# Performance work log

Hardware: AMD Instinct MI355X
Metric: run time of the kernel (lower is better)

## Reference

```python
import jax, jax.numpy as jnp
import numpy as np

NUM_BREAKPOINTS = 100  # module default
IMG_SHAPE = (1, 1, 4096, 8192)  # B must be 1: PWL(num_channels=1) sees (C*H*W, B)


def setup_inputs() -> dict:
    key = jax.random.key(0)
    k1, k2, k3, k4 = jax.random.split(key, 4)
    x = jax.random.uniform(k1, IMG_SHAPE, dtype=jnp.float32)
    # torchpwl.PWL parameters (num_channels=1): breakpoint x-positions, per-segment
    # slopes, and bias (function value at the leftmost breakpoint).
    x_positions = jax.random.uniform(k2, (1, NUM_BREAKPOINTS), dtype=jnp.float32)
    slopes = 1.0 + 0.1 * jax.random.normal(k3, (1, NUM_BREAKPOINTS), dtype=jnp.float32)
    biases = 0.05 * jax.random.normal(k4, (1,), dtype=jnp.float32)
    return {"x": x, "x_positions": x_positions, "slopes": slopes, "biases": biases}


def _pwl(x_flat, x_positions, slopes, biases):
    # Sloped piecewise-linear function (torchpwl.BaseSlopedPWL math), 1 channel.
    # x_flat: (N,), x_positions/slopes: (1, K), biases: (1,)
    K = x_positions.shape[1]
    sorted_x = jnp.sort(x_positions, axis=1)                     # (1, K)
    skips = jnp.roll(sorted_x, -1, axis=1) - sorted_x            # last entry never used
    cumsums = jnp.cumsum(skips * slopes, axis=1)[:, :-1]         # (1, K-1)
    betas = jnp.concatenate([biases[:, None], biases[:, None] + cumsums], axis=1)  # (1, K)
    # segment index: (# breakpoints <= x) clamped to [1, K], minus 1
    idx = jnp.clip(jnp.searchsorted(sorted_x[0], x_flat, side="right"), 1, K) - 1
    return betas[0, idx] + (x_flat - sorted_x[0, idx]) * slopes[0, idx]


def reference(x, x_positions, slopes, biases):
    # forward: flatten -> PWL -> clip(0,1) -> reshape (original returns [out])
    y = _pwl(x.reshape(-1), x_positions, slopes, biases)
    return jnp.clip(y, 0.0, 1.0).reshape(x.shape)
```

## Files before the change

### kernel.cpp

```cpp
#include <hip/hip_runtime.h>

#define K  100
#define NB 1024

typedef float fvec4 __attribute__((ext_vector_type(4)));

__global__ __launch_bounds__(1024) void pwl_setup_kernel(
    const float* __restrict__ xp, const float* __restrict__ sl,
    const float* __restrict__ bias, float2* __restrict__ bab_g,
    float* __restrict__ sx_g, float2* __restrict__ ab_g) {
  __shared__ float s_pos[K];
  __shared__ float s_slope[K];
  __shared__ float s_sorted[K];
  __shared__ float s_a[K];
  __shared__ float s_b[K];
  __shared__ unsigned short s_cnt[NB + 1];
  const int t = threadIdx.x;

  if (t < K) { s_pos[t] = xp[t]; s_slope[t] = sl[t]; }
  __syncthreads();

  if (t < K) {
    float v = s_pos[t];
    int r = 0;
    for (int j = 0; j < K; ++j) {
      float u = s_pos[j];
      r += ((u < v) || (u == v && j < t)) ? 1 : 0;
    }
    s_sorted[r] = v;
  }
  __syncthreads();

  if (t == 0) {
    float acc = bias[0];
    for (int i = 0; i < K; ++i) {
      if (i) acc += (s_sorted[i] - s_sorted[i - 1]) * s_slope[i - 1];
      float a = s_slope[i];
      s_a[i] = a;
      s_b[i] = acc - s_sorted[i] * a;
    }
  }
  __syncthreads();

  if (t < K) {
    sx_g[t] = s_sorted[t];
    ab_g[t] = make_float2(s_a[t], s_b[t]);
  }

  for (int e = t; e <= NB; e += blockDim.x) {
    float ev = (float)e * (1.0f / (float)NB);
    int c = 0;
    for (int j = 0; j < K; ++j) c += (s_sorted[j] <= ev) ? 1 : 0;
    s_cnt[e] = (unsigned short)c;
  }
  __syncthreads();

  for (int b = t; b < NB; b += blockDim.x) {
    int lo = s_cnt[b], hi = s_cnt[b + 1];
    float2 e;
    if (lo == hi) {
      int idx = min(max(lo, 1), K) - 1;
      e = make_float2(s_a[idx], s_b[idx]);
    } else {
      e.x = __builtin_huge_valf();
      e.y = __uint_as_float((unsigned)lo | ((unsigned)hi << 16));
    }
    bab_g[b] = e;
  }
}

__device__ __forceinline__ float pwl_eval(float xv,
                                          const float2* __restrict__ s_bab,
                                          const float* __restrict__ s_x,
                                          const float2* __restrict__ s_ab) {
  int b = (int)(xv * (float)NB);
  b = min(max(b, 0), NB - 1);
  float2 ab = s_bab[b];
  if (__float_as_uint(ab.x) == 0x7f800000u) {
    unsigned p = __float_as_uint(ab.y);
    int lo = (int)(p & 0xffffu);
    int hi = (int)(p >> 16);
    while (lo < hi) {
      int mid = (lo + hi) >> 1;
      if (s_x[mid] <= xv) lo = mid + 1; else hi = mid;
    }
    int idx = min(max(lo, 1), K) - 1;
    ab = s_ab[idx];
  }
  float y = fmaf(xv, ab.x, ab.y);
  return fminf(fmaxf(y, 0.0f), 1.0f);
}

__global__ __launch_bounds__(256) void pwl_main_kernel(
    const fvec4* __restrict__ x, const float2* __restrict__ bab_g,
    const float* __restrict__ sx_g, const float2* __restrict__ ab_g,
    fvec4* __restrict__ out, int n4, int n) {
  __shared__ float2 s_bab[NB];
  __shared__ float s_x[K];
  __shared__ float2 s_ab[K];
  for (int i = threadIdx.x; i < NB; i += blockDim.x) s_bab[i] = bab_g[i];
  if (threadIdx.x < K) {
    s_x[threadIdx.x] = sx_g[threadIdx.x];
    s_ab[threadIdx.x] = ab_g[threadIdx.x];
  }
  __syncthreads();

  const int stride = gridDim.x * blockDim.x;
  int i = blockIdx.x * blockDim.x + threadIdx.x;
  if (i < n4) {
    fvec4 v = __builtin_nontemporal_load(&x[i]);
    while (true) {
      int inext = i + stride;
      bool more = inext < n4;
      fvec4 vn = {};
      if (more) vn = __builtin_nontemporal_load(&x[inext]);
      fvec4 r;
      r.x = pwl_eval(v.x, s_bab, s_x, s_ab);
      r.y = pwl_eval(v.y, s_bab, s_x, s_ab);
      r.z = pwl_eval(v.z, s_bab, s_x, s_ab);
      r.w = pwl_eval(v.w, s_bab, s_x, s_ab);
      __builtin_nontemporal_store(r, &out[i]);
      if (!more) break;
      v = vn;
      i = inext;
    }
  }

  if (blockIdx.x == 0) {
    const float* xs = (const float*)x;
    float* os = (float*)out;
    for (int j = (n4 << 2) + threadIdx.x; j < n; j += blockDim.x) {
      os[j] = pwl_eval(xs[j], s_bab, s_x, s_ab);
    }
  }
}

extern "C" void kernel_launch(void* const* d_in, const int* in_sizes, int n_in,
                              void* d_out, int out_size, void* d_ws, size_t ws_size,
                              hipStream_t stream) {
  const float* x    = (const float*)d_in[0];
  const float* xp   = (const float*)d_in[1];
  const float* sl   = (const float*)d_in[2];
  const float* bias = (const float*)d_in[3];
  float* out = (float*)d_out;

  float2* bab = (float2*)d_ws;
  float* sx   = (float*)((char*)d_ws + NB * 8);
  float2* ab  = (float2*)((char*)d_ws + NB * 8 + 512);

  const int n  = in_sizes[0];
  const int n4 = n >> 2;

  pwl_setup_kernel<<<1, 1024, 0, stream>>>(xp, sl, bias, bab, sx, ab);

  const int threads = 256;
  const int blocks  = 2048;
  pwl_main_kernel<<<blocks, threads, 0, stream>>>(
      (const fvec4*)x, bab, sx, ab, (fvec4*)out, n4, n);
}
```

Baseline: 238.8 us.

## Fuse PWL table setup into main kernel, recomputed per block

Removes the separate single-block setup kernel. Each block of the main kernel now sorts the breakpoints, builds the bucket table in shared memory and then streams the data. The serial prefix sum is replaced by a parallel scan, and the bucket counting uses binary search instead of a linear scan. The launch changes to 1024 blocks of 512 threads. This saves a kernel launch and its dependency gap, but every block repeats the setup work before it starts streaming.

```diff
diff --git a/kernel.cpp b/kernel.cpp
--- a/kernel.cpp
+++ b/kernel.cpp
@@ -1,73 +1,11 @@
 #include <hip/hip_runtime.h>
 
-#define K  100
-#define NB 1024
+#define K   100
+#define NB  1024
+#define BS  512
+#define NBLK 1024
 
 typedef float fvec4 __attribute__((ext_vector_type(4)));
-
-__global__ __launch_bounds__(1024) void pwl_setup_kernel(
-    const float* __restrict__ xp, const float* __restrict__ sl,
-    const float* __restrict__ bias, float2* __restrict__ bab_g,
-    float* __restrict__ sx_g, float2* __restrict__ ab_g) {
-  __shared__ float s_pos[K];
-  __shared__ float s_slope[K];
-  __shared__ float s_sorted[K];
-  __shared__ float s_a[K];
-  __shared__ float s_b[K];
-  __shared__ unsigned short s_cnt[NB + 1];
-  const int t = threadIdx.x;
-
-  if (t < K) { s_pos[t] = xp[t]; s_slope[t] = sl[t]; }
-  __syncthreads();
-
-  if (t < K) {
-    float v = s_pos[t];
-    int r = 0;
-    for (int j = 0; j < K; ++j) {
-      float u = s_pos[j];
-      r += ((u < v) || (u == v && j < t)) ? 1 : 0;
-    }
-    s_sorted[r] = v;
-  }
-  __syncthreads();
-
-  if (t == 0) {
-    float acc = bias[0];
-    for (int i = 0; i < K; ++i) {
-      if (i) acc += (s_sorted[i] - s_sorted[i - 1]) * s_slope[i - 1];
-      float a = s_slope[i];
-      s_a[i] = a;
-      s_b[i] = acc - s_sorted[i] * a;
-    }
-  }
-  __syncthreads();
-
-  if (t < K) {
-    sx_g[t] = s_sorted[t];
-    ab_g[t] = make_float2(s_a[t], s_b[t]);
-  }
-
-  for (int e = t; e <= NB; e += blockDim.x) {
-    float ev = (float)e * (1.0f / (float)NB);
-    int c = 0;
-    for (int j = 0; j < K; ++j) c += (s_sorted[j] <= ev) ? 1 : 0;
-    s_cnt[e] = (unsigned short)c;
-  }
-  __syncthreads();
-
-  for (int b = t; b < NB; b += blockDim.x) {
-    int lo = s_cnt[b], hi = s_cnt[b + 1];
-    float2 e;
-    if (lo == hi) {
-      int idx = min(max(lo, 1), K) - 1;
-      e = make_float2(s_a[idx], s_b[idx]);
-    } else {
-      e.x = __builtin_huge_valf();
-      e.y = __uint_as_float((unsigned)lo | ((unsigned)hi << 16));
-    }
-    bab_g[b] = e;
-  }
-}
 
 __device__ __forceinline__ float pwl_eval(float xv,
                                           const float2* __restrict__ s_bab,
@@ -91,22 +29,77 @@
   return fminf(fmaxf(y, 0.0f), 1.0f);
 }
 
-__global__ __launch_bounds__(256) void pwl_main_kernel(
-    const fvec4* __restrict__ x, const float2* __restrict__ bab_g,
-    const float* __restrict__ sx_g, const float2* __restrict__ ab_g,
+__global__ __launch_bounds__(BS) void pwl_fused_kernel(
+    const fvec4* __restrict__ x, const float* __restrict__ xp,
+    const float* __restrict__ sl, const float* __restrict__ bias,
     fvec4* __restrict__ out, int n4, int n) {
+  __shared__ float s_pos[K];
+  __shared__ float s_slope[K];
+  __shared__ float s_x[K];
+  __shared__ float s_c[K];
+  __shared__ float2 s_ab[K];
+  __shared__ unsigned short s_cnt[NB + 1];
   __shared__ float2 s_bab[NB];
-  __shared__ float s_x[K];
-  __shared__ float2 s_ab[K];
-  for (int i = threadIdx.x; i < NB; i += blockDim.x) s_bab[i] = bab_g[i];
-  if (threadIdx.x < K) {
-    s_x[threadIdx.x] = sx_g[threadIdx.x];
-    s_ab[threadIdx.x] = ab_g[threadIdx.x];
+
+  const int t = threadIdx.x;
+
+  if (t < K) { s_pos[t] = xp[t]; s_slope[t] = sl[t]; }
+  __syncthreads();
+
+  if (t < K) {
+    float v = s_pos[t];
+    int r = 0;
+    for (int j = 0; j < K; ++j) {
+      float u = s_pos[j];
+      r += ((u < v) || (u == v && j < t)) ? 1 : 0;
+    }
+    s_x[r] = v;
   }
   __syncthreads();
 
-  const int stride = gridDim.x * blockDim.x;
-  int i = blockIdx.x * blockDim.x + threadIdx.x;
+  if (t < K - 1) s_c[t] = (s_x[t + 1] - s_x[t]) * s_slope[t];
+  __syncthreads();
+  for (int off = 1; off < K - 1; off <<= 1) {
+    float v = 0.0f;
+    if (t >= off && t < K - 1) v = s_c[t - off];
+    __syncthreads();
+    if (t < K - 1) s_c[t] += v;
+    __syncthreads();
+  }
+  if (t < K) {
+    float beta = bias[0] + (t ? s_c[t - 1] : 0.0f);
+    float a = s_slope[t];
+    s_ab[t] = make_float2(a, beta - s_x[t] * a);
+  }
+  __syncthreads();
+
+  for (int e = t; e <= NB; e += BS) {
+    float ev = (float)e * (1.0f / (float)NB);
+    int lo = 0, hi = K;
+    while (lo < hi) {
+      int mid = (lo + hi) >> 1;
+      if (s_x[mid] <= ev) lo = mid + 1; else hi = mid;
+    }
+    s_cnt[e] = (unsigned short)lo;
+  }
+  __syncthreads();
+
+  for (int b = t; b < NB; b += BS) {
+    int lo = s_cnt[b], hi = s_cnt[b + 1];
+    float2 e;
+    if (lo == hi) {
+      int idx = min(max(lo, 1), K) - 1;
+      e = s_ab[idx];
+    } else {
+      e.x = __builtin_huge_valf();
+      e.y = __uint_as_float((unsigned)lo | ((unsigned)hi << 16));
+    }
+    s_bab[b] = e;
+  }
+  __syncthreads();
+
+  const int stride = NBLK * BS;
+  int i = blockIdx.x * BS + t;
   if (i < n4) {
     fvec4 v = __builtin_nontemporal_load(&x[i]);
     while (true) {
@@ -129,7 +122,7 @@
   if (blockIdx.x == 0) {
     const float* xs = (const float*)x;
     float* os = (float*)out;
-    for (int j = (n4 << 2) + threadIdx.x; j < n; j += blockDim.x) {
+    for (int j = (n4 << 2) + t; j < n; j += BS) {
       os[j] = pwl_eval(xs[j], s_bab, s_x, s_ab);
     }
   }
@@ -144,17 +137,9 @@
   const float* bias = (const float*)d_in[3];
   float* out = (float*)d_out;
 
-  float2* bab = (float2*)d_ws;
-  float* sx   = (float*)((char*)d_ws + NB * 8);
-  float2* ab  = (float2*)((char*)d_ws + NB * 8 + 512);
-
   const int n  = in_sizes[0];
   const int n4 = n >> 2;
 
-  pwl_setup_kernel<<<1, 1024, 0, stream>>>(xp, sl, bias, bab, sx, ab);
-
-  const int threads = 256;
-  const int blocks  = 2048;
-  pwl_main_kernel<<<blocks, threads, 0, stream>>>(
-      (const fvec4*)x, bab, sx, ab, (fvec4*)out, n4, n);
+  pwl_fused_kernel<<<NBLK, BS, 0, stream>>>(
+      (const fvec4*)x, xp, sl, bias, (fvec4*)out, n4, n);
 }
```

After: 247.4 us. +3.6%, slower.

## Process eight elements per iteration with batched LUT lookups and parallel setup scan

Applied to the files above, without the earlier changes.

The main kernel now handles two float4 vectors per iteration, prefetching the next pair. It issues all eight bucket-table loads before checking which elements need a binary search, so LDS latency overlaps and the slow path is entered only when at least one element falls in a multi-breakpoint bucket. The setup kernel replaces its serial prefix sum with a parallel Hillis-Steele scan and its linear bucket count with a binary search. Input loads become regular loads instead of nontemporal ones, and launch bounds request higher occupancy, which could raise register pressure.

```diff
diff --git a/kernel.cpp b/kernel.cpp
--- a/kernel.cpp
+++ b/kernel.cpp
@@ -11,9 +11,10 @@
     float* __restrict__ sx_g, float2* __restrict__ ab_g) {
   __shared__ float s_pos[K];
   __shared__ float s_slope[K];
-  __shared__ float s_sorted[K];
-  __shared__ float s_a[K];
-  __shared__ float s_b[K];
+  __shared__ float s_x[K];
+  __shared__ float s_c[K];
+  __shared__ float s_sa[K];
+  __shared__ float s_sb[K];
   __shared__ unsigned short s_cnt[NB + 1];
   const int t = threadIdx.x;
 
@@ -27,31 +28,40 @@
       float u = s_pos[j];
       r += ((u < v) || (u == v && j < t)) ? 1 : 0;
     }
-    s_sorted[r] = v;
-  }
-  __syncthreads();
-
-  if (t == 0) {
-    float acc = bias[0];
-    for (int i = 0; i < K; ++i) {
-      if (i) acc += (s_sorted[i] - s_sorted[i - 1]) * s_slope[i - 1];
-      float a = s_slope[i];
-      s_a[i] = a;
-      s_b[i] = acc - s_sorted[i] * a;
-    }
-  }
-  __syncthreads();
-
+    s_x[r] = v;
+  }
+  __syncthreads();
+
+  if (t < K - 1) s_c[t] = (s_x[t + 1] - s_x[t]) * s_slope[t];
+  __syncthreads();
+  for (int off = 1; off < K - 1; off <<= 1) {
+    float v = 0.0f;
+    if (t >= off && t < K - 1) v = s_c[t - off];
+    __syncthreads();
+    if (t < K - 1) s_c[t] += v;
+    __syncthreads();
+  }
   if (t < K) {
-    sx_g[t] = s_sorted[t];
-    ab_g[t] = make_float2(s_a[t], s_b[t]);
+    float beta = bias[0] + (t ? s_c[t - 1] : 0.0f);
+    float a = s_slope[t];
+    s_sa[t] = a;
+    s_sb[t] = beta - s_x[t] * a;
+  }
+  __syncthreads();
+
+  if (t < K) {
+    sx_g[t] = s_x[t];
+    ab_g[t] = make_float2(s_sa[t], s_sb[t]);
   }
 
   for (int e = t; e <= NB; e += blockDim.x) {
     float ev = (float)e * (1.0f / (float)NB);
-    int c = 0;
-    for (int j = 0; j < K; ++j) c += (s_sorted[j] <= ev) ? 1 : 0;
-    s_cnt[e] = (unsigned short)c;
+    int lo = 0, hi = K;
+    while (lo < hi) {
+      int mid = (lo + hi) >> 1;
+      if (s_x[mid] <= ev) lo = mid + 1; else hi = mid;
+    }
+    s_cnt[e] = (unsigned short)lo;
   }
   __syncthreads();
 
@@ -60,7 +70,7 @@
     float2 e;
     if (lo == hi) {
       int idx = min(max(lo, 1), K) - 1;
-      e = make_float2(s_a[idx], s_b[idx]);
+      e = make_float2(s_sa[idx], s_sb[idx]);
     } else {
       e.x = __builtin_huge_valf();
       e.y = __uint_as_float((unsigned)lo | ((unsigned)hi << 16));
@@ -69,29 +79,7 @@
   }
 }
 
-__device__ __forceinline__ float pwl_eval(float xv,
-                                          const float2* __restrict__ s_bab,
-                                          const float* __restrict__ s_x,
-                                          const float2* __restrict__ s_ab) {
-  int b = (int)(xv * (float)NB);
-  b = min(max(b, 0), NB - 1);
-  float2 ab = s_bab[b];
-  if (__float_as_uint(ab.x) == 0x7f800000u) {
-    unsigned p = __float_as_uint(ab.y);
-    int lo = (int)(p & 0xffffu);
-    int hi = (int)(p >> 16);
-    while (lo < hi) {
-      int mid = (lo + hi) >> 1;
-      if (s_x[mid] <= xv) lo = mid + 1; else hi = mid;
-    }
-    int idx = min(max(lo, 1), K) - 1;
-    ab = s_ab[idx];
-  }
-  float y = fmaf(xv, ab.x, ab.y);
-  return fminf(fmaxf(y, 0.0f), 1.0f);
-}
-
-__global__ __launch_bounds__(256) void pwl_main_kernel(
+__global__ __launch_bounds__(256, 8) void pwl_main_kernel(
     const fvec4* __restrict__ x, const float2* __restrict__ bab_g,
     const float* __restrict__ sx_g, const float2* __restrict__ ab_g,
     fvec4* __restrict__ out, int n4, int n) {
@@ -106,31 +94,92 @@
   __syncthreads();
 
   const int stride = gridDim.x * blockDim.x;
-  int i = blockIdx.x * blockDim.x + threadIdx.x;
-  if (i < n4) {
-    fvec4 v = __builtin_nontemporal_load(&x[i]);
-    while (true) {
-      int inext = i + stride;
-      bool more = inext < n4;
-      fvec4 vn = {};
-      if (more) vn = __builtin_nontemporal_load(&x[inext]);
-      fvec4 r;
-      r.x = pwl_eval(v.x, s_bab, s_x, s_ab);
-      r.y = pwl_eval(v.y, s_bab, s_x, s_ab);
-      r.z = pwl_eval(v.z, s_bab, s_x, s_ab);
-      r.w = pwl_eval(v.w, s_bab, s_x, s_ab);
-      __builtin_nontemporal_store(r, &out[i]);
-      if (!more) break;
-      v = vn;
-      i = inext;
-    }
+  int i0 = blockIdx.x * blockDim.x + threadIdx.x;
+  int i1 = i0 + stride;
+  bool h0 = i0 < n4;
+  bool h1 = i1 < n4;
+  fvec4 v0 = {}, v1 = {};
+  if (h0) v0 = x[i0];
+  if (h1) v1 = x[i1];
+
+  while (h0) {
+    int j0 = i0 + 2 * stride;
+    int j1 = i1 + 2 * stride;
+    bool g0 = j0 < n4;
+    bool g1 = j1 < n4;
+    fvec4 w0 = {}, w1 = {};
+    if (g0) w0 = x[j0];
+    if (g1) w1 = x[j1];
+
+    float xe[8];
+    xe[0] = v0.x; xe[1] = v0.y; xe[2] = v0.z; xe[3] = v0.w;
+    xe[4] = v1.x; xe[5] = v1.y; xe[6] = v1.z; xe[7] = v1.w;
+
+    float2 ab[8];
+#pragma unroll
+    for (int e = 0; e < 8; ++e) {
+      int b = (int)(xe[e] * (float)NB);
+      b = min(max(b, 0), NB - 1);
+      ab[e] = s_bab[b];
+    }
+
+    unsigned dirty = 0;
+#pragma unroll
+    for (int e = 0; e < 8; ++e)
+      dirty |= (__float_as_uint(ab[e].x) == 0x7f800000u) ? (1u << e) : 0u;
+
+    if (dirty) {
+#pragma unroll
+      for (int e = 0; e < 8; ++e) {
+        if (dirty & (1u << e)) {
+          unsigned p = __float_as_uint(ab[e].y);
+          int lo = (int)(p & 0xffffu);
+          int hi = (int)(p >> 16);
+          while (lo < hi) {
+            int mid = (lo + hi) >> 1;
+            if (s_x[mid] <= xe[e]) lo = mid + 1; else hi = mid;
+          }
+          int idx = min(max(lo, 1), K) - 1;
+          ab[e] = s_ab[idx];
+        }
+      }
+    }
+
+    float y[8];
+#pragma unroll
+    for (int e = 0; e < 8; ++e)
+      y[e] = fminf(fmaxf(fmaf(xe[e], ab[e].x, ab[e].y), 0.0f), 1.0f);
+
+    fvec4 r0, r1;
+    r0.x = y[0]; r0.y = y[1]; r0.z = y[2]; r0.w = y[3];
+    r1.x = y[4]; r1.y = y[5]; r1.z = y[6]; r1.w = y[7];
+    __builtin_nontemporal_store(r0, &out[i0]);
+    if (h1) __builtin_nontemporal_store(r1, &out[i1]);
+
+    i0 = j0; i1 = j1;
+    v0 = w0; v1 = w1;
+    h0 = g0; h1 = g1;
   }
 
   if (blockIdx.x == 0) {
     const float* xs = (const float*)x;
     float* os = (float*)out;
     for (int j = (n4 << 2) + threadIdx.x; j < n; j += blockDim.x) {
-      os[j] = pwl_eval(xs[j], s_bab, s_x, s_ab);
+      float xv = xs[j];
+      int b = min(max((int)(xv * (float)NB), 0), NB - 1);
+      float2 ab = s_bab[b];
+      if (__float_as_uint(ab.x) == 0x7f800000u) {
+        unsigned p = __float_as_uint(ab.y);
+        int lo = (int)(p & 0xffffu);
+        int hi = (int)(p >> 16);
+        while (lo < hi) {
+          int mid = (lo + hi) >> 1;
+          if (s_x[mid] <= xv) lo = mid + 1; else hi = mid;
+        }
+        int idx = min(max(lo, 1), K) - 1;
+        ab = s_ab[idx];
+      }
+      os[j] = fminf(fmaxf(fmaf(xv, ab.x, ab.y), 0.0f), 1.0f);
     }
   }
 }
```

After: 251.2 us. 1.05x slower.

## Parallelize setup prefix sum and bucket search, drop nontemporal memory hints

Applied to the files above, without the earlier changes.

The single-thread serial cumulative sum in the setup kernel becomes a parallel Hillis-Steele scan across the first threads. The linear count per bucket edge becomes a binary search over the sorted breakpoints. The main kernel uses ordinary loads and stores in place of nontemporal ones. The intent is to shorten the serial setup kernel and to let the main streaming pass use default cache behaviour, though the scan changes floating-point summation order slightly.

```diff
diff --git a/kernel.cpp b/kernel.cpp
--- a/kernel.cpp
+++ b/kernel.cpp
@@ -11,9 +11,10 @@
     float* __restrict__ sx_g, float2* __restrict__ ab_g) {
   __shared__ float s_pos[K];
   __shared__ float s_slope[K];
-  __shared__ float s_sorted[K];
-  __shared__ float s_a[K];
-  __shared__ float s_b[K];
+  __shared__ float s_x[K];
+  __shared__ float s_c[K];
+  __shared__ float s_sa[K];
+  __shared__ float s_sb[K];
   __shared__ unsigned short s_cnt[NB + 1];
   const int t = threadIdx.x;
 
@@ -27,31 +28,40 @@
       float u = s_pos[j];
       r += ((u < v) || (u == v && j < t)) ? 1 : 0;
     }
-    s_sorted[r] = v;
+    s_x[r] = v;
   }
   __syncthreads();
 
-  if (t == 0) {
-    float acc = bias[0];
-    for (int i = 0; i < K; ++i) {
-      if (i) acc += (s_sorted[i] - s_sorted[i - 1]) * s_slope[i - 1];
-      float a = s_slope[i];
-      s_a[i] = a;
-      s_b[i] = acc - s_sorted[i] * a;
-    }
+  if (t < K - 1) s_c[t] = (s_x[t + 1] - s_x[t]) * s_slope[t];
+  __syncthreads();
+  for (int off = 1; off < K - 1; off <<= 1) {
+    float v = 0.0f;
+    if (t >= off && t < K - 1) v = s_c[t - off];
+    __syncthreads();
+    if (t < K - 1) s_c[t] += v;
+    __syncthreads();
+  }
+  if (t < K) {
+    float beta = bias[0] + (t ? s_c[t - 1] : 0.0f);
+    float a = s_slope[t];
+    s_sa[t] = a;
+    s_sb[t] = beta - s_x[t] * a;
   }
   __syncthreads();
 
   if (t < K) {
-    sx_g[t] = s_sorted[t];
-    ab_g[t] = make_float2(s_a[t], s_b[t]);
+    sx_g[t] = s_x[t];
+    ab_g[t] = make_float2(s_sa[t], s_sb[t]);
   }
 
   for (int e = t; e <= NB; e += blockDim.x) {
     float ev = (float)e * (1.0f / (float)NB);
-    int c = 0;
-    for (int j = 0; j < K; ++j) c += (s_sorted[j] <= ev) ? 1 : 0;
-    s_cnt[e] = (unsigned short)c;
+    int lo = 0, hi = K;
+    while (lo < hi) {
+      int mid = (lo + hi) >> 1;
+      if (s_x[mid] <= ev) lo = mid + 1; else hi = mid;
+    }
+    s_cnt[e] = (unsigned short)lo;
   }
   __syncthreads();
 
@@ -60,7 +70,7 @@
     float2 e;
     if (lo == hi) {
       int idx = min(max(lo, 1), K) - 1;
-      e = make_float2(s_a[idx], s_b[idx]);
+      e = make_float2(s_sa[idx], s_sb[idx]);
     } else {
       e.x = __builtin_huge_valf();
       e.y = __uint_as_float((unsigned)lo | ((unsigned)hi << 16));
@@ -108,18 +118,18 @@
   const int stride = gridDim.x * blockDim.x;
   int i = blockIdx.x * blockDim.x + threadIdx.x;
   if (i < n4) {
-    fvec4 v = __builtin_nontemporal_load(&x[i]);
+    fvec4 v = x[i];
     while (true) {
       int inext = i + stride;
       bool more = inext < n4;
       fvec4 vn = {};
-      if (more) vn = __builtin_nontemporal_load(&x[inext]);
+      if (more) vn = x[inext];
       fvec4 r;
       r.x = pwl_eval(v.x, s_bab, s_x, s_ab);
       r.y = pwl_eval(v.y, s_bab, s_x, s_ab);
       r.z = pwl_eval(v.z, s_bab, s_x, s_ab);
       r.w = pwl_eval(v.w, s_bab, s_x, s_ab);
-      __builtin_nontemporal_store(r, &out[i]);
+      out[i] = r;
       if (!more) break;
       v = vn;
       i = inext;
```

Result: no change. 241.2 us (+1.0%).
